# Optimization experiments

Measured on AMD Instinct MI355X. Metric: run time of the kernel, lower is better.

The kernel has to match this reference:

```python
import jax, jax.numpy as jnp
import numpy as np

NUM_HEADS = 32
HEAD_DIM = 128
HIDDEN = NUM_HEADS * HEAD_DIM  # 4096
ROPE_BASE = 10000.0
VISION_TOKEN_TYPE = 1


def vision_expert_mask(token_type_ids):
    # vision_token_mask[:, :-1] = (tt[:, :-1]==1) & (tt[:, 1:]==1); last col False
    tt = token_type_ids
    m = (tt[:, :-1] == VISION_TOKEN_TYPE) & (tt[:, 1:] == VISION_TOKEN_TYPE)
    return jnp.concatenate([m, jnp.zeros((tt.shape[0], 1), dtype=bool)], axis=1)


def rotary_cos_sin(position_ids, head_dim, dtype):
    inv_freq = 1.0 / (ROPE_BASE ** (jnp.arange(0, head_dim, 2, dtype=jnp.float32) / head_dim))
    freqs = position_ids.astype(jnp.float32)[..., None] * inv_freq  # [B,S,Dh/2]
    emb = jnp.concatenate([freqs, freqs], axis=-1)  # [B,S,Dh]
    return jnp.cos(emb).astype(dtype), jnp.sin(emb).astype(dtype)


def rotate_half(x):
    d = x.shape[-1] // 2
    return jnp.concatenate([-x[..., d:], x[..., :d]], axis=-1)


def setup_inputs() -> dict:
    key = jax.random.key(0)
    ks = jax.random.split(key, 5)
    B, S = 2, 2048
    hidden_states = jax.random.normal(ks[0], (B, S, HIDDEN), dtype=jnp.float32)
    token_type_ids = jax.random.randint(ks[1], (B, S), 0, 2, dtype=jnp.int64)
    position_ids = jnp.broadcast_to(jnp.arange(S, dtype=jnp.int64)[None, :], (B, S))
    scale = 0.02
    w_vis_qkv = jax.random.normal(ks[2], (HIDDEN, 3 * HIDDEN), dtype=jnp.float32) * scale
    w_lang_qkv = jax.random.normal(ks[3], (HIDDEN, 3 * HIDDEN), dtype=jnp.float32) * scale
    w_vis_dense = jax.random.normal(ks[4], (HIDDEN, HIDDEN), dtype=jnp.float32) * scale
    w_lang_dense = jax.random.normal(jax.random.fold_in(key, 7), (HIDDEN, HIDDEN), dtype=jnp.float32) * scale
    return dict(hidden_states=hidden_states, token_type_ids=token_type_ids,
                position_ids=position_ids, w_vis_qkv=w_vis_qkv, w_lang_qkv=w_lang_qkv,
                w_vis_dense=w_vis_dense, w_lang_dense=w_lang_dense)


def reference(hidden_states, token_type_ids, position_ids,
              w_vis_qkv, w_lang_qkv, w_vis_dense, w_lang_dense):
    B, S, D = hidden_states.shape
    vm = vision_expert_mask(token_type_ids)  # [B,S] bool

    # 2-expert QKV dispatch (mask-select between the two expert GEMMs)
    qkv = jnp.where(vm[..., None],
                    hidden_states @ w_vis_qkv,
                    hidden_states @ w_lang_qkv)  # [B,S,3D]
    q, k, v = jnp.split(qkv, 3, axis=-1)
    q = q.reshape(B, S, NUM_HEADS, HEAD_DIM)
    k = k.reshape(B, S, NUM_HEADS, HEAD_DIM)
    v = v.reshape(B, S, NUM_HEADS, HEAD_DIM)

    # rotary embedding on q, k
    cos, sin = rotary_cos_sin(position_ids, HEAD_DIM, q.dtype)  # [B,S,Dh]
    cos, sin = cos[:, :, None, :], sin[:, :, None, :]
    q = q * cos + rotate_half(q) * sin
    k = k * cos + rotate_half(k) * sin

    # causal attention (dense equivalent of the paged-attention call)
    scores = jnp.einsum('bqhd,bkhd->bhqk', q, k) / jnp.sqrt(jnp.array(HEAD_DIM, q.dtype))
    causal = jnp.tril(jnp.ones((S, S), dtype=bool))
    scores = jnp.where(causal[None, None], scores, jnp.finfo(scores.dtype).min)
    probs = jax.nn.softmax(scores, axis=-1)
    ctx = jnp.einsum('bhqk,bkhd->bqhd', probs, v).reshape(B, S, D)

    # 2-expert output dense dispatch
    attn_output = jnp.where(vm[..., None],
                            ctx @ w_vis_dense,
                            ctx @ w_lang_dense)
    return attn_output
```

## Files before the change

kernel.cpp:

```cpp
#include <hip/hip_runtime.h>
#include <math.h>

#define SEQ     2048
#define NB      2
#define NHEADS  32
#define DHEAD   128
#define HID     4096
#define NQKV    12288
#define T_TOKENS (NB*SEQ)

typedef _Float16 half8 __attribute__((ext_vector_type(8)));
typedef float v4f __attribute__((ext_vector_type(4)));

__device__ __forceinline__ void gload_lds16(const void* g, void* l) {
    __builtin_amdgcn_global_load_lds(
        (__attribute__((address_space(1))) void*)(void*)(g),
        (__attribute__((address_space(3))) void*)(unsigned)(unsigned long long)(l),
        16, 0, 0);
}

__device__ __forceinline__ v4f mfma16(half8 a, half8 b, v4f c) {
    return __builtin_amdgcn_mfma_f32_16x16x32_f16(a, b, c, 0, 0, 0);
}

__global__ void route_kernel(const int* __restrict__ tt, int* counts, int* idx) {
    int t = blockIdx.x * blockDim.x + threadIdx.x;
    if (t >= T_TOKENS) return;
    int s = t & (SEQ - 1);
    bool vm = (s < SEQ - 1) && (tt[t] == 1) && (tt[t + 1] == 1);
    int e = vm ? 0 : 1;
    int p = atomicAdd(&counts[e], 1);
    idx[e * T_TOKENS + p] = t;
}

__global__ void rope_table_kernel(const int* __restrict__ pos_ids, float2* __restrict__ tab) {
    int i = blockIdx.x * blockDim.x + threadIdx.x;
    if (i >= T_TOKENS * 64) return;
    int tok = i >> 6, j = i & 63;
    float invf = (float)pow(10000.0, -(double)j * (1.0 / 64.0));
    float ang = (float)pos_ids[tok] * invf;
    double ds, dc;
    sincos((double)ang, &ds, &dc);
    tab[i] = make_float2((float)dc, (float)ds);
}

__global__ void cvt_f32_f16(const float* __restrict__ src, _Float16* __restrict__ dst, int n4) {
    int i = blockIdx.x * blockDim.x + threadIdx.x;
    if (i >= n4) return;
    float4 v = ((const float4*)src)[i];
    union { _Float16 h[4]; uint2 u; } p;
    p.h[0] = (_Float16)v.x; p.h[1] = (_Float16)v.y;
    p.h[2] = (_Float16)v.z; p.h[3] = (_Float16)v.w;
    ((uint2*)dst)[i] = p.u;
}

__global__ void transpose_cvt(const float* __restrict__ W, _Float16* __restrict__ WT,
                              int K, int N) {
    __shared__ _Float16 t[64][72];
    const int n0 = blockIdx.x * 64, k0 = blockIdx.y * 64;
    const int cr = threadIdx.x & 15, rr = threadIdx.x >> 4;
#pragma unroll
    for (int it = 0; it < 4; ++it) {
        int r = rr + it * 16;
        float4 v = *(const float4*)&W[(size_t)(k0 + r) * N + n0 + cr * 4];
        t[cr*4+0][r] = (_Float16)v.x; t[cr*4+1][r] = (_Float16)v.y;
        t[cr*4+2][r] = (_Float16)v.z; t[cr*4+3][r] = (_Float16)v.w;
    }
    __syncthreads();
#pragma unroll
    for (int it = 0; it < 4; ++it) {
        int r = rr + it * 16;
        union { _Float16 h[4]; uint2 u; } p;
#pragma unroll
        for (int j = 0; j < 4; ++j) p.h[j] = t[r][cr*4+j];
        *(uint2*)&WT[(size_t)(n0 + r) * K + k0 + cr * 4] = p.u;
    }
}

__global__ void transpose_v(const _Float16* __restrict__ vin, _Float16* __restrict__ vout) {
    __shared__ _Float16 t[64][72];
    const int s0 = blockIdx.x * 64;
    const int d0 = blockIdx.y * 64;
    const int bh = blockIdx.z;
    const int b = bh >> 5, h = bh & 31;
    const int cr = threadIdx.x & 15, rr = threadIdx.x >> 4;
#pragma unroll
    for (int it = 0; it < 4; ++it) {
        int sl = rr + it * 16;
        union { _Float16 h4[4]; uint2 u; } p;
        p.u = *(const uint2*)&vin[(size_t)(b * SEQ + s0 + sl) * HID + h * DHEAD + d0 + cr * 4];
#pragma unroll
        for (int j = 0; j < 4; ++j) t[cr*4+j][sl] = p.h4[j];
    }
    __syncthreads();
#pragma unroll
    for (int it = 0; it < 4; ++it) {
        int dl = rr + it * 16;
        union { _Float16 h4[4]; uint2 u; } p;
#pragma unroll
        for (int j = 0; j < 4; ++j) p.h4[j] = t[dl][cr*4+j];
        *(uint2*)&vout[((size_t)bh * DHEAD + d0 + dl) * SEQ + s0 + cr * 4] = p.u;
    }
}

template <int MODE, int NCT>
__global__ __launch_bounds__(256, 2)
void gemm_expert(const _Float16* __restrict__ A,
                 const _Float16* __restrict__ BT0,
                 const _Float16* __restrict__ BT1,
                 const int* __restrict__ counts,
                 const int* __restrict__ idx_all,
                 const float2* __restrict__ rope,
                 _Float16* __restrict__ qbuf,
                 _Float16* __restrict__ kbuf,
                 _Float16* __restrict__ vbuf,
                 float* __restrict__ out) {
    const int e = blockIdx.z;
    const int count = counts[e];

    const int f   = blockIdx.x + NCT * blockIdx.y;
    const int xcd = f & 7;
    const int g   = f >> 3;
    const int c   = g >> 6;
    const int wi  = g & 63;
    const int rt  = wi >> 1;
    const int ct  = xcd * (NCT / 8) + c * 2 + (wi & 1);

    if (rt * 128 >= count) return;
    const int* idx = idx_all + e * T_TOKENS;
    const _Float16* BT = e ? BT1 : BT0;

    __shared__ _Float16 sA[4][128 * 32];
    __shared__ _Float16 sB[4][128 * 32];

    const int tid = threadIdx.x;
    const int w = tid >> 6, lane = tid & 63;
    const int col = lane & 15, quad = lane >> 4;
    const int wm = w >> 1, wn = w & 1;

    const int r0 = (w * 2 + 0) * 16 + (lane >> 2);
    const int r1 = (w * 2 + 1) * 16 + (lane >> 2);
    int g0 = rt * 128 + r0; if (g0 > count - 1) g0 = count - 1;
    int g1 = rt * 128 + r1; if (g1 > count - 1) g1 = count - 1;
    const int tok0 = idx[g0], tok1 = idx[g1];
    const int schk = (lane & 3) ^ ((lane >> 3) & 3);
    const _Float16* ag0 = A + (size_t)tok0 * HID + schk * 8;
    const _Float16* ag1 = A + (size_t)tok1 * HID + schk * 8;
    const _Float16* bg0 = BT + (size_t)(ct * 128 + r0) * HID + schk * 8;
    const _Float16* bg1 = BT + (size_t)(ct * 128 + r1) * HID + schk * 8;
    const int sa_off0 = (w * 2 + 0) * 512;
    const int sa_off1 = (w * 2 + 1) * 512;

    v4f acc[4][4];
#pragma unroll
    for (int i = 0; i < 4; ++i)
#pragma unroll
        for (int j = 0; j < 4; ++j) { v4f z = {0.f, 0.f, 0.f, 0.f}; acc[i][j] = z; }

    const int kofq = (quad ^ ((col >> 1) & 3)) * 8;

    auto stage = [&](int buf) {
        gload_lds16(ag0, &sA[buf][sa_off0]); gload_lds16(ag1, &sA[buf][sa_off1]);
        gload_lds16(bg0, &sB[buf][sa_off0]); gload_lds16(bg1, &sB[buf][sa_off1]);
        ag0 += 32; ag1 += 32; bg0 += 32; bg1 += 32;
    };
    auto compute = [&](int cur) {
        half8 a[4], b[4];
#pragma unroll
        for (int i = 0; i < 4; ++i)
            a[i] = *(const half8*)&sA[cur][(wm * 64 + i * 16 + col) * 32 + kofq];
#pragma unroll
        for (int j = 0; j < 4; ++j)
            b[j] = *(const half8*)&sB[cur][((wn + 2 * j) * 16 + col) * 32 + kofq];
#pragma unroll
        for (int i = 0; i < 4; ++i)
#pragma unroll
            for (int j = 0; j < 4; ++j)
                acc[i][j] = mfma16(a[i], b[j], acc[i][j]);
    };

    const int NK = HID / 32;
    stage(0); stage(1); stage(2);

    for (int kt = 0; kt < NK - 3; ++kt) {
        asm volatile("s_waitcnt vmcnt(8)" ::: "memory");
        __builtin_amdgcn_s_barrier();
        asm volatile("" ::: "memory");
        stage((kt + 3) & 3);
        compute(kt & 3);
    }
    asm volatile("s_waitcnt vmcnt(8)" ::: "memory");
    __builtin_amdgcn_s_barrier();
    asm volatile("" ::: "memory");
    compute((NK - 3) & 3);
    asm volatile("s_waitcnt vmcnt(4)" ::: "memory");
    __builtin_amdgcn_s_barrier();
    asm volatile("" ::: "memory");
    compute((NK - 2) & 3);
    asm volatile("s_waitcnt vmcnt(0)" ::: "memory");
    __builtin_amdgcn_s_barrier();
    asm volatile("" ::: "memory");
    compute((NK - 1) & 3);

    const int n0 = ct * 128;
    if (MODE == 1) {
#pragma unroll
        for (int i = 0; i < 4; ++i)
#pragma unroll
            for (int r = 0; r < 4; ++r) {
                int rg = rt * 128 + wm * 64 + i * 16 + quad * 4 + r;
                if (rg >= count) continue;
                int tok = idx[rg];
                float* dst = out + (size_t)tok * HID + n0;
#pragma unroll
                for (int j = 0; j < 4; ++j) dst[(wn + 2 * j) * 16 + col] = acc[i][j][r];
            }
    } else {
        const int sec = n0 >> 12;
        const int h = (n0 >> 7) & 31;
#pragma unroll
        for (int i = 0; i < 4; ++i)
#pragma unroll
            for (int r = 0; r < 4; ++r) {
                int rg = rt * 128 + wm * 64 + i * 16 + quad * 4 + r;
                if (rg >= count) continue;
                int tok = idx[rg];
                int b = tok >> 11, s = tok & (SEQ - 1);
                if (sec == 2) {
                    _Float16* dst = vbuf + (size_t)tok * HID + h * DHEAD;
#pragma unroll
                    for (int j = 0; j < 4; ++j) dst[(wn + 2 * j) * 16 + col] = (_Float16)acc[i][j][r];
                } else {
                    _Float16* dst = (sec ? kbuf : qbuf) + ((size_t)(b * NHEADS + h) * SEQ + s) * DHEAD;
                    const float2* tp = rope + (size_t)tok * 64;
#pragma unroll
                    for (int j = 0; j < 2; ++j) {
                        int d = (wn + 2 * j) * 16 + col;
                        float2 cs = tp[d];
                        float x = acc[i][j][r], y = acc[i][j + 2][r];
                        dst[d]      = (_Float16)(x * cs.x - y * cs.y);
                        dst[d + 64] = (_Float16)(y * cs.x + x * cs.y);
                    }
                }
            }
    }
}

__global__ __launch_bounds__(256, 2)
void attn_kernel(const _Float16* __restrict__ qbuf,
                 const _Float16* __restrict__ kbuf,
                 const _Float16* __restrict__ vt,
                 _Float16* __restrict__ ctx) {
    const int f   = blockIdx.x;
    const int xcd = f & 7;
    const int t   = f >> 3;
    const int s   = t & 31;
    const int rr  = t >> 5;
    const int u   = s & 15, g = s >> 4;
    const int bh  = xcd * 8 + rr * 2 + g;
    const int qt  = (rr & 1) ? (15 - u) : u;

    const int b = bh >> 5, h = bh & 31;
    const int tid = threadIdx.x;
    const int w = tid >> 6, lane = tid & 63;
    const int col = lane & 15, quad = lane >> 4;

    __shared__ _Float16 sK[2][64 * 128];
    __shared__ _Float16 sV[2][128 * 64];
    __shared__ _Float16 sP[128 * 64];

    half8 qf[2][4];
    const _Float16 qscale = (_Float16)0.08838834764831845f;
#pragma unroll
    for (int mt = 0; mt < 2; ++mt)
#pragma unroll
        for (int kc = 0; kc < 4; ++kc) {
            int row = qt * 128 + w * 32 + mt * 16 + col;
            half8 v = *(const half8*)&qbuf[((size_t)bh * SEQ + row) * DHEAD + kc * 32 + quad * 8];
            qf[mt][kc] = v * qscale;
        }

    float mrow[2][4], lrow[2][4];
    v4f o[2][8];
#pragma unroll
    for (int mt = 0; mt < 2; ++mt)
#pragma unroll
        for (int r = 0; r < 4; ++r) { mrow[mt][r] = -3.0e38f; lrow[mt][r] = 0.f; }
#pragma unroll
    for (int i = 0; i < 2; ++i)
#pragma unroll
        for (int j = 0; j < 8; ++j) { v4f z = {0.f, 0.f, 0.f, 0.f}; o[i][j] = z; }

    const int cxor = col & 7;
    const int vs_chk = (lane & 7) ^ (lane >> 3);
    const int nkt = 2 * qt + 2;

    const _Float16* kg0 = kbuf + (size_t)bh * SEQ * DHEAD;
    const _Float16* vg0 = vt + (size_t)bh * DHEAD * SEQ;

    auto stage = [&](int kt, int buf) {
        const _Float16* kg = kg0 + (size_t)kt * 64 * DHEAD;
        const _Float16* vg = vg0 + kt * 64;
#pragma unroll
        for (int op = 0; op < 4; ++op) {
            int r0 = (w * 4 + op) * 4;
            int krow = r0 + quad;
            int kcs = col ^ (krow & 7);
            gload_lds16(kg + (size_t)krow * DHEAD + kcs * 8, &sK[buf][r0 * 128]);
            int d0 = (w * 4 + op) * 8;
            int vrow = d0 + (lane >> 3);
            gload_lds16(vg + (size_t)vrow * SEQ + vs_chk * 8, &sV[buf][d0 * 64]);
        }
    };

    stage(0, 0);
    __syncthreads();

    for (int kt = 0; kt < nkt; ++kt) {
        const int cur = kt & 1;
        if (kt + 1 < nkt) stage(kt + 1, cur ^ 1);

        v4f sc[2][4];
#pragma unroll
        for (int i = 0; i < 2; ++i)
#pragma unroll
            for (int j = 0; j < 4; ++j) { v4f z = {0.f, 0.f, 0.f, 0.f}; sc[i][j] = z; }
        __builtin_amdgcn_s_setprio(1);
#pragma unroll
        for (int kc = 0; kc < 4; ++kc) {
            const int kof = ((kc * 4 + quad) ^ cxor) * 8;
#pragma unroll
            for (int nt = 0; nt < 4; ++nt) {
                half8 bf = *(const half8*)&sK[cur][(size_t)(nt * 16 + col) * 128 + kof];
                sc[0][nt] = mfma16(qf[0][kc], bf, sc[0][nt]);
                sc[1][nt] = mfma16(qf[1][kc], bf, sc[1][nt]);
            }
        }
        __builtin_amdgcn_s_setprio(0);

        if (kt >= 2 * qt) {
#pragma unroll
            for (int mt = 0; mt < 2; ++mt)
#pragma unroll
                for (int nt = 0; nt < 4; ++nt)
#pragma unroll
                    for (int r = 0; r < 4; ++r) {
                        int rowa = qt * 128 + w * 32 + mt * 16 + quad * 4 + r;
                        int cola = kt * 64 + nt * 16 + col;
                        if (cola > rowa) sc[mt][nt][r] = -3.0e38f;
                    }
        }

#pragma unroll
        for (int mt = 0; mt < 2; ++mt)
#pragma unroll
            for (int r = 0; r < 4; ++r) {
                float mx = sc[mt][0][r];
#pragma unroll
                for (int nt = 1; nt < 4; ++nt) mx = fmaxf(mx, sc[mt][nt][r]);
                mx = fmaxf(mx, __shfl_xor(mx, 1));
                mx = fmaxf(mx, __shfl_xor(mx, 2));
                mx = fmaxf(mx, __shfl_xor(mx, 4));
                mx = fmaxf(mx, __shfl_xor(mx, 8));
                float newm = fmaxf(mrow[mt][r], mx);
                float alpha = __expf(mrow[mt][r] - newm);
                mrow[mt][r] = newm;
                float rs = 0.f;
#pragma unroll
                for (int nt = 0; nt < 4; ++nt) {
                    float p = __expf(sc[mt][nt][r] - newm);
                    sc[mt][nt][r] = p;
                    rs += p;
                }
                rs += __shfl_xor(rs, 1); rs += __shfl_xor(rs, 2);
                rs += __shfl_xor(rs, 4); rs += __shfl_xor(rs, 8);
                lrow[mt][r] = lrow[mt][r] * alpha + rs;
#pragma unroll
                for (int nt = 0; nt < 8; ++nt) o[mt][nt][r] *= alpha;
            }

#pragma unroll
        for (int mt = 0; mt < 2; ++mt)
#pragma unroll
            for (int nt = 0; nt < 4; ++nt)
#pragma unroll
                for (int r = 0; r < 4; ++r) {
                    int rp = w * 32 + mt * 16 + quad * 4 + r;
                    int colh = nt * 16 + col;
                    int c = (colh >> 3) ^ (rp & 7);
                    sP[(size_t)rp * 64 + c * 8 + (colh & 7)] = (_Float16)sc[mt][nt][r];
                }

        __builtin_amdgcn_s_setprio(1);
#pragma unroll
        for (int kc = 0; kc < 2; ++kc) {
            const int kof = ((kc * 4 + quad) ^ cxor) * 8;
            half8 p0 = *(const half8*)&sP[(size_t)(w * 32 + col) * 64 + kof];
            half8 p1 = *(const half8*)&sP[(size_t)(w * 32 + 16 + col) * 64 + kof];
#pragma unroll
            for (int nt = 0; nt < 8; ++nt) {
                half8 vf = *(const half8*)&sV[cur][(size_t)(nt * 16 + col) * 64 + kof];
                o[0][nt] = mfma16(p0, vf, o[0][nt]);
                o[1][nt] = mfma16(p1, vf, o[1][nt]);
            }
        }
        __builtin_amdgcn_s_setprio(0);

        __syncthreads();
    }

#pragma unroll
    for (int mt = 0; mt < 2; ++mt)
#pragma unroll
        for (int r = 0; r < 4; ++r) {
            int rowa = qt * 128 + w * 32 + mt * 16 + quad * 4 + r;
            float inv = 1.0f / lrow[mt][r];
            _Float16* dst = ctx + ((size_t)b * SEQ + rowa) * HID + h * DHEAD;
#pragma unroll
            for (int nt = 0; nt < 8; ++nt)
                dst[nt * 16 + col] = (_Float16)(o[mt][nt][r] * inv);
        }
}

extern "C" void kernel_launch(void* const* d_in, const int* in_sizes, int n_in,
                              void* d_out, int out_size, void* d_ws, size_t ws_size,
                              hipStream_t stream) {
    const float* hidden = (const float*)d_in[0];
    const int*   tt     = (const int*)d_in[1];
    const int*   pos    = (const int*)d_in[2];
    const float* wvq    = (const float*)d_in[3];
    const float* wlq    = (const float*)d_in[4];
    const float* wvd    = (const float*)d_in[5];
    const float* wld    = (const float*)d_in[6];
    float* out = (float*)d_out;

    char* ws = (char*)d_ws;
    size_t off = 0;
    auto alloc = [&](size_t bytes) {
        char* p = ws + off;
        off += (bytes + 255) & ~(size_t)255;
        return p;
    };
    const size_t TOKB = (size_t)T_TOKENS * HID * sizeof(_Float16);
    _Float16* h16  = (_Float16*)alloc(TOKB);
    _Float16* wvqT = (_Float16*)alloc((size_t)NQKV * HID * 2);
    _Float16* wlqT = (_Float16*)alloc((size_t)NQKV * HID * 2);
    _Float16* wvdT = (_Float16*)alloc((size_t)HID * HID * 2);
    _Float16* wldT = (_Float16*)alloc((size_t)HID * HID * 2);
    _Float16* qb   = (_Float16*)alloc(TOKB);
    _Float16* kb   = (_Float16*)alloc(TOKB);
    _Float16* vtmp = (_Float16*)alloc(TOKB);
    int* counts = (int*)alloc(2 * sizeof(int));
    int* idx    = (int*)alloc(2 * T_TOKENS * sizeof(int));
    float2* rope = (float2*)alloc((size_t)T_TOKENS * 64 * sizeof(float2));
    _Float16* vT  = h16;
    _Float16* ctx = vtmp;

    hipMemsetAsync(counts, 0, 2 * sizeof(int), stream);
    route_kernel<<<T_TOKENS / 256, 256, 0, stream>>>(tt, counts, idx);
    rope_table_kernel<<<(T_TOKENS * 64) / 256, 256, 0, stream>>>(pos, rope);
    cvt_f32_f16<<<(T_TOKENS * HID / 4) / 256, 256, 0, stream>>>(hidden, h16, T_TOKENS * HID / 4);
    transpose_cvt<<<dim3(NQKV / 64, HID / 64), 256, 0, stream>>>(wvq, wvqT, HID, NQKV);
    transpose_cvt<<<dim3(NQKV / 64, HID / 64), 256, 0, stream>>>(wlq, wlqT, HID, NQKV);
    transpose_cvt<<<dim3(HID / 64, HID / 64), 256, 0, stream>>>(wvd, wvdT, HID, HID);
    transpose_cvt<<<dim3(HID / 64, HID / 64), 256, 0, stream>>>(wld, wldT, HID, HID);
    gemm_expert<0, NQKV / 128><<<dim3(NQKV / 128, T_TOKENS / 128, 2), 256, 0, stream>>>(
        h16, wvqT, wlqT, counts, idx, rope, qb, kb, vtmp, nullptr);
    transpose_v<<<dim3(SEQ / 64, DHEAD / 64, NB * NHEADS), 256, 0, stream>>>(vtmp, vT);
    attn_kernel<<<dim3(16 * NB * NHEADS), 256, 0, stream>>>(qb, kb, vT, ctx);
    gemm_expert<1, HID / 128><<<dim3(HID / 128, T_TOKENS / 128, 2), 256, 0, stream>>>(
        ctx, wvdT, wldT, counts, idx, nullptr, nullptr, nullptr, nullptr, out);
}
```

Measured before the change: 1.535 ms.

## Enlarge expert GEMM tiles to 256x256 with 512-thread blocks

Doubles the expert GEMM block tile from 128x128 to 256x256 and uses 8 waves per block, each computing a 128x64 sub-tile with 8x4 MFMA accumulators. The aim is more data reuse per LDS load and less global traffic per FLOP. The epilogue is remapped so the rope pairing spans two heads per block column tile. In exchange, LDS use doubles to 128KB, register pressure rises, there are fewer blocks to fill the CUs, and padding waste grows for partially filled expert row tiles.

```diff
diff --git a/kernel.cpp b/kernel.cpp
--- a/kernel.cpp
+++ b/kernel.cpp
@@ -104,7 +104,7 @@
 }
 
 template <int MODE, int NCT>
-__global__ __launch_bounds__(256, 2)
+__global__ __launch_bounds__(512, 2)
 void gemm_expert(const _Float16* __restrict__ A,
                  const _Float16* __restrict__ BT0,
                  const _Float16* __restrict__ BT1,
@@ -121,59 +121,62 @@
     const int f   = blockIdx.x + NCT * blockIdx.y;
     const int xcd = f & 7;
     const int g   = f >> 3;
-    const int c   = g >> 6;
-    const int wi  = g & 63;
+    const int c   = g >> 5;
+    const int wi  = g & 31;
     const int rt  = wi >> 1;
     const int ct  = xcd * (NCT / 8) + c * 2 + (wi & 1);
 
-    if (rt * 128 >= count) return;
+    if (rt * 256 >= count) return;
     const int* idx = idx_all + e * T_TOKENS;
     const _Float16* BT = e ? BT1 : BT0;
 
-    __shared__ _Float16 sA[4][128 * 32];
-    __shared__ _Float16 sB[4][128 * 32];
+    __shared__ _Float16 sA[4][256 * 32];
+    __shared__ _Float16 sB[4][256 * 32];
 
     const int tid = threadIdx.x;
     const int w = tid >> 6, lane = tid & 63;
     const int col = lane & 15, quad = lane >> 4;
-    const int wm = w >> 1, wn = w & 1;
-
-    const int r0 = (w * 2 + 0) * 16 + (lane >> 2);
-    const int r1 = (w * 2 + 1) * 16 + (lane >> 2);
-    int g0 = rt * 128 + r0; if (g0 > count - 1) g0 = count - 1;
-    int g1 = rt * 128 + r1; if (g1 > count - 1) g1 = count - 1;
-    const int tok0 = idx[g0], tok1 = idx[g1];
+    const int wm = w >> 2, wn = w & 3;
+
     const int schk = (lane & 3) ^ ((lane >> 3) & 3);
-    const _Float16* ag0 = A + (size_t)tok0 * HID + schk * 8;
-    const _Float16* ag1 = A + (size_t)tok1 * HID + schk * 8;
-    const _Float16* bg0 = BT + (size_t)(ct * 128 + r0) * HID + schk * 8;
-    const _Float16* bg1 = BT + (size_t)(ct * 128 + r1) * HID + schk * 8;
-    const int sa_off0 = (w * 2 + 0) * 512;
-    const int sa_off1 = (w * 2 + 1) * 512;
-
-    v4f acc[4][4];
-#pragma unroll
-    for (int i = 0; i < 4; ++i)
+    const _Float16* ag[2];
+    const _Float16* bg[2];
+    int so[2];
+#pragma unroll
+    for (int o = 0; o < 2; ++o) {
+        int r = w * 32 + o * 16 + (lane >> 2);
+        int gg = rt * 256 + r; if (gg > count - 1) gg = count - 1;
+        ag[o] = A + (size_t)idx[gg] * HID + schk * 8;
+        bg[o] = BT + (size_t)(ct * 256 + r) * HID + schk * 8;
+        so[o] = (w * 32 + o * 16) * 32;
+    }
+
+    v4f acc[8][4];
+#pragma unroll
+    for (int i = 0; i < 8; ++i)
 #pragma unroll
         for (int j = 0; j < 4; ++j) { v4f z = {0.f, 0.f, 0.f, 0.f}; acc[i][j] = z; }
 
     const int kofq = (quad ^ ((col >> 1) & 3)) * 8;
 
     auto stage = [&](int buf) {
-        gload_lds16(ag0, &sA[buf][sa_off0]); gload_lds16(ag1, &sA[buf][sa_off1]);
-        gload_lds16(bg0, &sB[buf][sa_off0]); gload_lds16(bg1, &sB[buf][sa_off1]);
-        ag0 += 32; ag1 += 32; bg0 += 32; bg1 += 32;
+#pragma unroll
+        for (int o = 0; o < 2; ++o) {
+            gload_lds16(ag[o], &sA[buf][so[o]]);
+            gload_lds16(bg[o], &sB[buf][so[o]]);
+            ag[o] += 32; bg[o] += 32;
+        }
     };
     auto compute = [&](int cur) {
-        half8 a[4], b[4];
-#pragma unroll
-        for (int i = 0; i < 4; ++i)
-            a[i] = *(const half8*)&sA[cur][(wm * 64 + i * 16 + col) * 32 + kofq];
+        half8 a[8], b[4];
+#pragma unroll
+        for (int i = 0; i < 8; ++i)
+            a[i] = *(const half8*)&sA[cur][(wm * 128 + i * 16 + col) * 32 + kofq];
 #pragma unroll
         for (int j = 0; j < 4; ++j)
-            b[j] = *(const half8*)&sB[cur][((wn + 2 * j) * 16 + col) * 32 + kofq];
-#pragma unroll
-        for (int i = 0; i < 4; ++i)
+            b[j] = *(const half8*)&sB[cur][((4 * j + wn) * 16 + col) * 32 + kofq];
+#pragma unroll
+        for (int i = 0; i < 8; ++i)
 #pragma unroll
             for (int j = 0; j < 4; ++j)
                 acc[i][j] = mfma16(a[i], b[j], acc[i][j]);
@@ -202,42 +205,47 @@
     asm volatile("" ::: "memory");
     compute((NK - 1) & 3);
 
-    const int n0 = ct * 128;
+    const int n0 = ct * 256;
     if (MODE == 1) {
 #pragma unroll
-        for (int i = 0; i < 4; ++i)
+        for (int i = 0; i < 8; ++i)
 #pragma unroll
             for (int r = 0; r < 4; ++r) {
-                int rg = rt * 128 + wm * 64 + i * 16 + quad * 4 + r;
+                int rg = rt * 256 + wm * 128 + i * 16 + quad * 4 + r;
                 if (rg >= count) continue;
                 int tok = idx[rg];
                 float* dst = out + (size_t)tok * HID + n0;
 #pragma unroll
-                for (int j = 0; j < 4; ++j) dst[(wn + 2 * j) * 16 + col] = acc[i][j][r];
+                for (int j = 0; j < 4; ++j) dst[(4 * j + wn) * 16 + col] = acc[i][j][r];
             }
     } else {
         const int sec = n0 >> 12;
-        const int h = (n0 >> 7) & 31;
-#pragma unroll
-        for (int i = 0; i < 4; ++i)
+        const int h0 = (n0 >> 7) & 31;
+#pragma unroll
+        for (int i = 0; i < 8; ++i)
 #pragma unroll
             for (int r = 0; r < 4; ++r) {
-                int rg = rt * 128 + wm * 64 + i * 16 + quad * 4 + r;
+                int rg = rt * 256 + wm * 128 + i * 16 + quad * 4 + r;
                 if (rg >= count) continue;
                 int tok = idx[rg];
                 int b = tok >> 11, s = tok & (SEQ - 1);
                 if (sec == 2) {
-                    _Float16* dst = vbuf + (size_t)tok * HID + h * DHEAD;
-#pragma unroll
-                    for (int j = 0; j < 4; ++j) dst[(wn + 2 * j) * 16 + col] = (_Float16)acc[i][j][r];
+#pragma unroll
+                    for (int j = 0; j < 4; ++j) {
+                        int h = (h0 + (j >> 1)) & 31;
+                        vbuf[(size_t)tok * HID + h * DHEAD + (j & 1) * 64 + wn * 16 + col] =
+                            (_Float16)acc[i][j][r];
+                    }
                 } else {
-                    _Float16* dst = (sec ? kbuf : qbuf) + ((size_t)(b * NHEADS + h) * SEQ + s) * DHEAD;
                     const float2* tp = rope + (size_t)tok * 64;
-#pragma unroll
-                    for (int j = 0; j < 2; ++j) {
-                        int d = (wn + 2 * j) * 16 + col;
-                        float2 cs = tp[d];
-                        float x = acc[i][j][r], y = acc[i][j + 2][r];
+                    int d = wn * 16 + col;
+                    float2 cs = tp[d];
+#pragma unroll
+                    for (int jj = 0; jj < 4; jj += 2) {
+                        int h = (h0 + (jj >> 1)) & 31;
+                        _Float16* dst = (sec ? kbuf : qbuf) +
+                            ((size_t)(b * NHEADS + h) * SEQ + s) * DHEAD;
+                        float x = acc[i][jj][r], y = acc[i][jj + 1][r];
                         dst[d]      = (_Float16)(x * cs.x - y * cs.y);
                         dst[d + 64] = (_Float16)(y * cs.x + x * cs.y);
                     }
@@ -464,10 +472,10 @@
     transpose_cvt<<<dim3(NQKV / 64, HID / 64), 256, 0, stream>>>(wlq, wlqT, HID, NQKV);
     transpose_cvt<<<dim3(HID / 64, HID / 64), 256, 0, stream>>>(wvd, wvdT, HID, HID);
     transpose_cvt<<<dim3(HID / 64, HID / 64), 256, 0, stream>>>(wld, wldT, HID, HID);
-    gemm_expert<0, NQKV / 128><<<dim3(NQKV / 128, T_TOKENS / 128, 2), 256, 0, stream>>>(
+    gemm_expert<0, NQKV / 256><<<dim3(NQKV / 256, T_TOKENS / 256, 2), 512, 0, stream>>>(
         h16, wvqT, wlqT, counts, idx, rope, qb, kb, vtmp, nullptr);
     transpose_v<<<dim3(SEQ / 64, DHEAD / 64, NB * NHEADS), 256, 0, stream>>>(vtmp, vT);
     attn_kernel<<<dim3(16 * NB * NHEADS), 256, 0, stream>>>(qb, kb, vT, ctx);
-    gemm_expert<1, HID / 128><<<dim3(HID / 128, T_TOKENS / 128, 2), 256, 0, stream>>>(
+    gemm_expert<1, HID / 256><<<dim3(HID / 256, T_TOKENS / 256, 2), 512, 0, stream>>>(
         ctx, wvdT, wldT, counts, idx, nullptr, nullptr, nullptr, nullptr, out);
 }
```

Result: no change. 1.535 ms (-0.0%).
